# Performance work log

Measured on AMD Instinct MI355X. Metric: run time of the kernel, lower is better.

The kernel has to match this reference:

```python
import jax, jax.numpy as jnp
import numpy as np

B, S, H, D = 2, 2048, 16, 64
HID = H * D
THETA = 10000.0
SCALING_FACTOR = 1
NEG_INF = -1e9


def _rope_cos_sin(position_ids):
    # Llama RoPE: inv_freq over even dims, duplicated halves.
    inv_freq = 1.0 / (THETA ** (jnp.arange(0, D, 2, dtype=jnp.float32) / D))  # [D/2]
    freqs = position_ids.astype(jnp.float32)[..., None] * inv_freq            # [B,S,D/2]
    emb = jnp.concatenate([freqs, freqs], axis=-1)                            # [B,S,D]
    return jnp.cos(emb), jnp.sin(emb)


def _rotate_half(x):
    x1, x2 = jnp.split(x, 2, axis=-1)
    return jnp.concatenate([-x2, x1], axis=-1)


def setup_inputs() -> dict:
    key = jax.random.key(0)
    ks = jax.random.split(key, 6)
    return {
        "hidden_states": jax.random.normal(ks[0], (B, S, HID), dtype=jnp.float32),
        "info_embeddings": jax.random.normal(ks[1], (B, S, HID), dtype=jnp.float32) * 0.1,
        "Wq": jax.random.normal(ks[2], (HID, HID), dtype=jnp.float32) * 0.02,
        "Wk": jax.random.normal(ks[3], (HID, HID), dtype=jnp.float32) * 0.02,
        "Wv": jax.random.normal(ks[4], (HID, HID), dtype=jnp.float32) * 0.02,
        "Wo": jax.random.normal(ks[5], (HID, HID), dtype=jnp.float32) * 0.02,
        "position_ids": jnp.broadcast_to(jnp.arange(S, dtype=jnp.int64), (B, S)),
    }


def reference(hidden_states, info_embeddings, Wq, Wk, Wv, Wo, position_ids):
    b, s, _ = hidden_states.shape
    # projections -> [B,H,S,D]
    q = (hidden_states @ Wq).reshape(b, s, H, D).transpose(0, 2, 1, 3)
    k = (hidden_states @ Wk).reshape(b, s, H, D).transpose(0, 2, 1, 3)
    v = (hidden_states @ Wv).reshape(b, s, H, D).transpose(0, 2, 1, 3)
    # info embedding added to q and k (pre-RoPE)
    info = info_embeddings.reshape(b, s, H, D).transpose(0, 2, 1, 3)
    q = q + info
    k = k + info
    # rotary position embedding
    cos, sin = _rope_cos_sin(position_ids)
    cos = cos[:, None]  # [B,1,S,D]
    sin = sin[:, None]
    q = q * cos + _rotate_half(q) * sin
    k = k * cos + _rotate_half(k) * sin
    # eager attention with custom scaling
    scale = 1.0 / float(np.sqrt(SCALING_FACTOR * D))
    scores = jnp.einsum("bhqd,bhkd->bhqk", q, k) * scale  # [B,H,S,S]
    causal = jnp.tril(jnp.ones((s, s), dtype=bool))
    scores = scores + jnp.where(causal, 0.0, NEG_INF).astype(scores.dtype)
    probs = jax.nn.softmax(scores, axis=-1)  # dropout p=0 (eval)
    attn = jnp.einsum("bhqk,bhkd->bhqd", probs, v)
    attn = attn.transpose(0, 2, 1, 3).reshape(b, s, HID)
    return attn @ Wo
```

## Files before the change

### kernel.cpp

```cpp
#include <hip/hip_runtime.h>
#include <hip/hip_bf16.h>

#define HB 2
#define HS 2048
#define HH 16
#define HD 64
#define HIDN 1024
#define MROWS 4096

typedef __attribute__((ext_vector_type(8))) short s16x8;
typedef __attribute__((ext_vector_type(4))) float f32x4;
typedef unsigned short u16;

__device__ inline u16 f2bf(float f) {
  union { __hip_bfloat16 h; u16 u; } cvt;
  cvt.h = __float2bfloat16(f);
  return cvt.u;
}

__device__ __forceinline__ void gload16(const u16* g, u16* l) {
  __builtin_amdgcn_global_load_lds((const __attribute__((address_space(1))) void*)g,
                                   (__attribute__((address_space(3))) void*)l, 16, 0, 0);
}

__global__ __launch_bounds__(256) void k_cvt(const float* __restrict__ in, u16* __restrict__ out, int n) {
  int i = (blockIdx.x * 256 + threadIdx.x) * 4;
  if (i >= n) return;
  float4 a = *(const float4*)(in + i);
  ushort4 r;
  r.x = f2bf(a.x); r.y = f2bf(a.y); r.z = f2bf(a.z); r.w = f2bf(a.w);
  *(ushort4*)(out + i) = r;
}

__global__ __launch_bounds__(256) void k_transpose(const float* __restrict__ W0, const float* __restrict__ W1,
                                                   const float* __restrict__ W2, const float* __restrict__ W3,
                                                   u16* __restrict__ out) {
  const float* W = (blockIdx.z == 0) ? W0 : (blockIdx.z == 1) ? W1 : (blockIdx.z == 2) ? W2 : W3;
  u16* O = out + (size_t)blockIdx.z * HIDN * HIDN;
  __shared__ float tile[64][65];
  int k0 = blockIdx.y * 64, c0 = blockIdx.x * 64;
  #pragma unroll
  for (int i = 0; i < 16; ++i) {
    int id = threadIdx.x + i * 256;
    int r = id >> 6, c = id & 63;
    tile[r][c] = W[(size_t)(k0 + r) * HIDN + c0 + c];
  }
  __syncthreads();
  #pragma unroll
  for (int i = 0; i < 16; ++i) {
    int id = threadIdx.x + i * 256;
    int r = id >> 6, c = id & 63;
    O[(size_t)(c0 + r) * HIDN + k0 + c] = f2bf(tile[c][r]);
  }
}

#define BM 128
#define BN 128
#define BK 64
#define LDK 72

__global__ __launch_bounds__(256) void k_qkv(const u16* __restrict__ X, const u16* __restrict__ Wt,
                                             const float* __restrict__ info,
                                             u16* __restrict__ Qb, u16* __restrict__ Kb, u16* __restrict__ Vt) {
  __shared__ __align__(16) u16 smem[128 * 136];
  const int z = blockIdx.z;
  const u16* Bt = Wt + (size_t)z * HIDN * HIDN;
  const int tid = threadIdx.x;
  const int lane = tid & 63, wave = tid >> 6;
  const int wr = wave >> 1, wc = wave & 1;
  const int lg = lane >> 4, li = lane & 15;
  const int bm0 = blockIdx.y * BM, bn0 = blockIdx.x * BN;

  const int srow = lane >> 3;
  const int scol = (lane & 7) * 8;

  f32x4 acc[4][4];
  #pragma unroll
  for (int m = 0; m < 4; ++m)
    #pragma unroll
    for (int n = 0; n < 4; ++n) acc[m][n] = (f32x4){0.f, 0.f, 0.f, 0.f};

  for (int k0 = 0; k0 < HIDN; k0 += BK) {
    __syncthreads();
    #pragma unroll
    for (int c = 0; c < 4; ++c) {
      const int ci = wave * 4 + c;
      const int row = ci * 8 + srow;
      gload16(X  + (size_t)(bm0 + row) * HIDN + k0 + scol, &smem[ci * 512]);
      gload16(Bt + (size_t)(bn0 + row) * HIDN + k0 + scol, &smem[8192 + ci * 512]);
    }
    __syncthreads();
    #pragma unroll
    for (int kk = 0; kk < 2; ++kk) {
      s16x8 af[4], bfr[4];
      #pragma unroll
      for (int m = 0; m < 4; ++m) af[m]  = *(const s16x8*)(&smem[(wr * 64 + m * 16 + li) * 64 + kk * 32 + lg * 8]);
      #pragma unroll
      for (int n = 0; n < 4; ++n) bfr[n] = *(const s16x8*)(&smem[8192 + (wc * 64 + n * 16 + li) * 64 + kk * 32 + lg * 8]);
      __builtin_amdgcn_s_setprio(1);
      #pragma unroll
      for (int m = 0; m < 4; ++m)
        #pragma unroll
        for (int n = 0; n < 4; ++n)
          acc[m][n] = __builtin_amdgcn_mfma_f32_16x16x32_bf16(af[m], bfr[n], acc[m][n], 0, 0, 0);
      __builtin_amdgcn_s_setprio(0);
    }
  }

  if (z < 2) {
    u16* dst = (z == 0) ? Qb : Kb;
    #pragma unroll
    for (int m = 0; m < 4; ++m) {
      #pragma unroll
      for (int r = 0; r < 4; ++r) {
        int t = bm0 + wr * 64 + m * 16 + lg * 4 + r;
        int b = t >> 11, s = t & (HS - 1);
        #pragma unroll
        for (int n = 0; n < 2; ++n) {
          int c1 = bn0 + wc * 64 + n * 16 + li;
          float v1 = acc[m][n][r]     + info[(size_t)t * HIDN + c1];
          float v2 = acc[m][n + 2][r] + info[(size_t)t * HIDN + c1 + 32];
          int j = n * 16 + li;
          float invf = exp2f(-0.41524101186092030f * (float)j);
          float ang = (float)s * invf;
          float sn, cs;
          __sincosf(ang, &sn, &cs);
          float o1 = v1 * cs - v2 * sn;
          float o2 = v2 * cs + v1 * sn;
          if (z == 0) { o1 *= 0.18033688011f; o2 *= 0.18033688011f; }
          int h = c1 >> 6, d1 = c1 & 63;
          size_t base = ((size_t)(b * HH + h) * HS + s) * HD;
          dst[base + d1]      = f2bf(o1);
          dst[base + d1 + 32] = f2bf(o2);
        }
      }
    }
  } else {
    __syncthreads();
    #pragma unroll
    for (int m = 0; m < 4; ++m)
      #pragma unroll
      for (int n = 0; n < 4; ++n)
        #pragma unroll
        for (int r = 0; r < 4; ++r) {
          int cl = wc * 64 + n * 16 + li;
          int ml = wr * 64 + m * 16 + lg * 4 + r;
          smem[cl * 136 + ml] = f2bf(acc[m][n][r]);
        }
    __syncthreads();
    const int b = bm0 >> 11, s0 = bm0 & (HS - 1);
    #pragma unroll
    for (int p = 0; p < 8; ++p) {
      int id = tid + p * 256;
      int cl = id >> 4, m8 = (id & 15) * 8;
      int c = bn0 + cl;
      int h = c >> 6, d = c & 63;
      s16x8 v = *(const s16x8*)(&smem[cl * 136 + m8]);
      *(s16x8*)(&Vt[((size_t)(b * HH + h) * HD + d) * HS + s0 + m8]) = v;
    }
  }
}

__global__ __launch_bounds__(512, 4) void k_attn(const u16* __restrict__ Qb, const u16* __restrict__ Kb,
                                                 const u16* __restrict__ Vt, u16* __restrict__ attnOut) {
  __shared__ u16 Ks[2][64 * LDK];
  __shared__ u16 Vs[2][64 * LDK];
  __shared__ u16 Ps[8][16 * LDK];
  const int bidx = blockIdx.x;
  const int bh = bidx & 31;
  const int x  = bidx >> 5;
  const int j  = (x < 8) ? x : 23 - x;
  const int q0 = j * 128;
  const int ntiles = 2 * j + 2;

  const u16* Qh = Qb + (size_t)bh * HS * HD;
  const u16* Kh = Kb + (size_t)bh * HS * HD;
  const u16* Vh = Vt + (size_t)bh * HD * HS;
  const int tid = threadIdx.x;
  const int lane = tid & 63, w = tid >> 6;
  const int lg = lane >> 4, li = lane & 15;
  const int b = bh >> 4, h = bh & 15;

  const int row8 = lane >> 3;
  const int col8 = (lane & 7) * 8;

  s16x8 qf[2];
  #pragma unroll
  for (int kk = 0; kk < 2; ++kk)
    qf[kk] = *(const s16x8*)(Qh + (size_t)(q0 + w * 16 + li) * HD + kk * 32 + lg * 8);

  f32x4 o[4];
  #pragma unroll
  for (int n = 0; n < 4; ++n) o[n] = (f32x4){0.f, 0.f, 0.f, 0.f};
  float mrow = -3e38f, lrow = 0.f;

  {
    uint4 rK = *(const uint4*)(Kh + (size_t)(w * 8 + row8) * HD + col8);
    uint4 rV = *(const uint4*)(Vh + (size_t)(w * 8 + row8) * HS + col8);
    *(uint4*)(&Ks[0][(w * 8 + row8) * LDK + col8]) = rK;
    *(uint4*)(&Vs[0][(w * 8 + row8) * LDK + col8]) = rV;
  }
  __syncthreads();

  for (int t = 0; t < ntiles; ++t) {
    const int cur = t & 1;
    uint4 rK, rV;
    const bool more = (t + 1 < ntiles);
    if (more) {
      const int kv1 = (t + 1) * 64;
      rK = *(const uint4*)(Kh + (size_t)(kv1 + w * 8 + row8) * HD + col8);
      rV = *(const uint4*)(Vh + (size_t)(w * 8 + row8) * HS + kv1 + col8);
    }

    f32x4 sc[4];
    #pragma unroll
    for (int n = 0; n < 4; ++n) sc[n] = (f32x4){0.f, 0.f, 0.f, 0.f};
    __builtin_amdgcn_s_setprio(1);
    #pragma unroll
    for (int kk = 0; kk < 2; ++kk) {
      #pragma unroll
      for (int n = 0; n < 4; ++n) {
        s16x8 kfr = *(const s16x8*)(&Ks[cur][(n * 16 + li) * LDK + kk * 32 + lg * 8]);
        sc[n] = __builtin_amdgcn_mfma_f32_16x16x32_bf16(kfr, qf[kk], sc[n], 0, 0, 0);
      }
    }
    __builtin_amdgcn_s_setprio(0);

    if (t >= 2 * j) {
      const int qglob = q0 + w * 16 + li;
      #pragma unroll
      for (int n = 0; n < 4; ++n)
        #pragma unroll
        for (int r = 0; r < 4; ++r)
          if (t * 64 + n * 16 + lg * 4 + r > qglob) sc[n][r] = -1e9f;
    }

    float pmax = sc[0][0];
    #pragma unroll
    for (int n = 0; n < 4; ++n)
      #pragma unroll
      for (int r = 0; r < 4; ++r) pmax = fmaxf(pmax, sc[n][r]);
    pmax = fmaxf(pmax, __shfl_xor(pmax, 16));
    pmax = fmaxf(pmax, __shfl_xor(pmax, 32));

    if (!__all(pmax - mrow <= 11.5f)) {
      float mnew = fmaxf(mrow, pmax);
      float corr = exp2f(mrow - mnew);
      mrow = mnew;
      lrow *= corr;
      float corrq[4];
      #pragma unroll
      for (int r = 0; r < 4; ++r) corrq[r] = __shfl(corr, lg * 4 + r);
      #pragma unroll
      for (int n = 0; n < 4; ++n)
        #pragma unroll
        for (int r = 0; r < 4; ++r) o[n][r] *= corrq[r];
    }

    float psum = 0.f;
    #pragma unroll
    for (int n = 0; n < 4; ++n) {
      u16 pb[4];
      #pragma unroll
      for (int r = 0; r < 4; ++r) {
        float p = exp2f(sc[n][r] - mrow);
        psum += p;
        pb[r] = f2bf(p);
      }
      uint2 wv;
      wv.x = (unsigned)pb[0] | ((unsigned)pb[1] << 16);
      wv.y = (unsigned)pb[2] | ((unsigned)pb[3] << 16);
      *(uint2*)(&Ps[w][li * LDK + n * 16 + lg * 4]) = wv;
    }
    psum += __shfl_xor(psum, 16);
    psum += __shfl_xor(psum, 32);
    lrow += psum;

    __builtin_amdgcn_s_setprio(1);
    #pragma unroll
    for (int kk = 0; kk < 2; ++kk) {
      s16x8 pf = *(const s16x8*)(&Ps[w][li * LDK + kk * 32 + lg * 8]);
      #pragma unroll
      for (int n = 0; n < 4; ++n) {
        s16x8 vf = *(const s16x8*)(&Vs[cur][(n * 16 + li) * LDK + kk * 32 + lg * 8]);
        o[n] = __builtin_amdgcn_mfma_f32_16x16x32_bf16(pf, vf, o[n], 0, 0, 0);
      }
    }
    __builtin_amdgcn_s_setprio(0);

    if (more) {
      *(uint4*)(&Ks[cur ^ 1][(w * 8 + row8) * LDK + col8]) = rK;
      *(uint4*)(&Vs[cur ^ 1][(w * 8 + row8) * LDK + col8]) = rV;
      __syncthreads();
    }
  }

  float linv = 1.0f / lrow;
  float linvq[4];
  #pragma unroll
  for (int r = 0; r < 4; ++r) linvq[r] = __shfl(linv, lg * 4 + r);
  #pragma unroll
  for (int n = 0; n < 4; ++n)
    #pragma unroll
    for (int r = 0; r < 4; ++r) {
      int srow = q0 + w * 16 + lg * 4 + r;
      attnOut[(size_t)(b * HS + srow) * HIDN + h * 64 + n * 16 + li] = f2bf(o[n][r] * linvq[r]);
    }
}

__global__ __launch_bounds__(256) void k_out(const u16* __restrict__ A, const u16* __restrict__ Bt,
                                             float* __restrict__ out) {
  __shared__ __align__(16) u16 As[BM * 64];
  __shared__ __align__(16) u16 Bs[BN * 64];
  const int tid = threadIdx.x;
  const int lane = tid & 63, wave = tid >> 6;
  const int wr = wave >> 1, wc = wave & 1;
  const int lg = lane >> 4, li = lane & 15;
  const int bm0 = blockIdx.y * BM, bn0 = blockIdx.x * BN;

  const int srow = lane >> 3;
  const int scol = (lane & 7) * 8;

  f32x4 acc[4][4];
  #pragma unroll
  for (int m = 0; m < 4; ++m)
    #pragma unroll
    for (int n = 0; n < 4; ++n) acc[m][n] = (f32x4){0.f, 0.f, 0.f, 0.f};

  for (int k0 = 0; k0 < HIDN; k0 += BK) {
    __syncthreads();
    #pragma unroll
    for (int c = 0; c < 4; ++c) {
      const int ci = wave * 4 + c;
      const int row = ci * 8 + srow;
      gload16(A  + (size_t)(bm0 + row) * HIDN + k0 + scol, &As[ci * 512]);
      gload16(Bt + (size_t)(bn0 + row) * HIDN + k0 + scol, &Bs[ci * 512]);
    }
    __syncthreads();
    #pragma unroll
    for (int kk = 0; kk < 2; ++kk) {
      s16x8 af[4], bfr[4];
      #pragma unroll
      for (int m = 0; m < 4; ++m) af[m]  = *(const s16x8*)(&As[(wr * 64 + m * 16 + li) * 64 + kk * 32 + lg * 8]);
      #pragma unroll
      for (int n = 0; n < 4; ++n) bfr[n] = *(const s16x8*)(&Bs[(wc * 64 + n * 16 + li) * 64 + kk * 32 + lg * 8]);
      __builtin_amdgcn_s_setprio(1);
      #pragma unroll
      for (int m = 0; m < 4; ++m)
        #pragma unroll
        for (int n = 0; n < 4; ++n)
          acc[m][n] = __builtin_amdgcn_mfma_f32_16x16x32_bf16(af[m], bfr[n], acc[m][n], 0, 0, 0);
      __builtin_amdgcn_s_setprio(0);
    }
  }

  #pragma unroll
  for (int m = 0; m < 4; ++m)
    #pragma unroll
    for (int r = 0; r < 4; ++r) {
      int t = bm0 + wr * 64 + m * 16 + lg * 4 + r;
      #pragma unroll
      for (int n = 0; n < 4; ++n) {
        int c = bn0 + wc * 64 + n * 16 + li;
        out[(size_t)t * HIDN + c] = acc[m][n][r];
      }
    }
}

extern "C" void kernel_launch(void* const* d_in, const int* in_sizes, int n_in,
                              void* d_out, int out_size, void* d_ws, size_t ws_size,
                              hipStream_t stream) {
  const float* hs   = (const float*)d_in[0];
  const float* info = (const float*)d_in[1];
  const float* Wq   = (const float*)d_in[2];
  const float* Wk   = (const float*)d_in[3];
  const float* Wv   = (const float*)d_in[4];
  const float* Wo   = (const float*)d_in[5];
  float* out = (float*)d_out;

  char* ws = (char*)d_ws;
  u16* Xbf  = (u16*)(ws);
  u16* Wt   = (u16*)(ws + ((size_t)8  << 20));
  u16* Qb   = (u16*)(ws + ((size_t)16 << 20));
  u16* Kb   = (u16*)(ws + ((size_t)24 << 20));
  u16* Vt   = (u16*)(ws + ((size_t)32 << 20));
  u16* attn = Xbf;

  k_cvt<<<(MROWS * HIDN / 4 + 255) / 256, 256, 0, stream>>>(hs, Xbf, MROWS * HIDN);
  k_transpose<<<dim3(16, 16, 4), 256, 0, stream>>>(Wq, Wk, Wv, Wo, Wt);
  k_qkv<<<dim3(HIDN / BN, MROWS / BM, 3), 256, 0, stream>>>(Xbf, Wt, info, Qb, Kb, Vt);
  k_attn<<<dim3(512), 512, 0, stream>>>(Qb, Kb, Vt, attn);
  k_out<<<dim3(HIDN / BN, MROWS / BM), 256, 0, stream>>>(attn, Wt + (size_t)3 * HIDN * HIDN, out);
}
```

Before: 129.2 us.

## Split attention into 64-row query blocks with 256 threads, heaviest-first ordering

The attention kernel now uses 256-thread blocks, each covering 64 query rows, with 1024 blocks launched in descending-work order in place of the paired 128-row scheme. Each thread loads two K and V rows per tile, and the causal mask applies only to the diagonal tile. The fp32-to-bf16 conversion of probabilities is replaced by a round-half-up add plus a byte permute. This aims at better load balance and occupancy across CUs. The cost is K/V tiles being reloaded by twice as many blocks, and slightly different rounding, since ties and NaN are not handled like round-to-nearest-even.

```diff
diff --git a/kernel.cpp b/kernel.cpp
--- a/kernel.cpp
+++ b/kernel.cpp
@@ -161,17 +161,16 @@
   }
 }
 
-__global__ __launch_bounds__(512, 4) void k_attn(const u16* __restrict__ Qb, const u16* __restrict__ Kb,
+__global__ __launch_bounds__(256, 3) void k_attn(const u16* __restrict__ Qb, const u16* __restrict__ Kb,
                                                  const u16* __restrict__ Vt, u16* __restrict__ attnOut) {
   __shared__ u16 Ks[2][64 * LDK];
   __shared__ u16 Vs[2][64 * LDK];
-  __shared__ u16 Ps[8][16 * LDK];
+  __shared__ u16 Ps[4][16 * LDK];
   const int bidx = blockIdx.x;
   const int bh = bidx & 31;
-  const int x  = bidx >> 5;
-  const int j  = (x < 8) ? x : 23 - x;
-  const int q0 = j * 128;
-  const int ntiles = 2 * j + 2;
+  const int j  = 31 - (bidx >> 5);
+  const int q0 = j * 64;
+  const int ntiles = j + 1;
 
   const u16* Qh = Qb + (size_t)bh * HS * HD;
   const u16* Kh = Kb + (size_t)bh * HS * HD;
@@ -181,8 +180,8 @@
   const int lg = lane >> 4, li = lane & 15;
   const int b = bh >> 4, h = bh & 15;
 
-  const int row8 = lane >> 3;
-  const int col8 = (lane & 7) * 8;
+  const int row16 = tid >> 3;
+  const int col8  = (tid & 7) * 8;
 
   s16x8 qf[2];
   #pragma unroll
@@ -195,21 +194,27 @@
   float mrow = -3e38f, lrow = 0.f;
 
   {
-    uint4 rK = *(const uint4*)(Kh + (size_t)(w * 8 + row8) * HD + col8);
-    uint4 rV = *(const uint4*)(Vh + (size_t)(w * 8 + row8) * HS + col8);
-    *(uint4*)(&Ks[0][(w * 8 + row8) * LDK + col8]) = rK;
-    *(uint4*)(&Vs[0][(w * 8 + row8) * LDK + col8]) = rV;
+    uint4 ka = *(const uint4*)(Kh + (size_t)row16 * HD + col8);
+    uint4 kb = *(const uint4*)(Kh + (size_t)(row16 + 32) * HD + col8);
+    uint4 va = *(const uint4*)(Vh + (size_t)row16 * HS + col8);
+    uint4 vb = *(const uint4*)(Vh + (size_t)(row16 + 32) * HS + col8);
+    *(uint4*)(&Ks[0][row16 * LDK + col8])        = ka;
+    *(uint4*)(&Ks[0][(row16 + 32) * LDK + col8]) = kb;
+    *(uint4*)(&Vs[0][row16 * LDK + col8])        = va;
+    *(uint4*)(&Vs[0][(row16 + 32) * LDK + col8]) = vb;
   }
   __syncthreads();
 
   for (int t = 0; t < ntiles; ++t) {
     const int cur = t & 1;
-    uint4 rK, rV;
+    uint4 rKa, rKb, rVa, rVb;
     const bool more = (t + 1 < ntiles);
     if (more) {
       const int kv1 = (t + 1) * 64;
-      rK = *(const uint4*)(Kh + (size_t)(kv1 + w * 8 + row8) * HD + col8);
-      rV = *(const uint4*)(Vh + (size_t)(w * 8 + row8) * HS + kv1 + col8);
+      rKa = *(const uint4*)(Kh + (size_t)(kv1 + row16) * HD + col8);
+      rKb = *(const uint4*)(Kh + (size_t)(kv1 + row16 + 32) * HD + col8);
+      rVa = *(const uint4*)(Vh + (size_t)row16 * HS + kv1 + col8);
+      rVb = *(const uint4*)(Vh + (size_t)(row16 + 32) * HS + kv1 + col8);
     }
 
     f32x4 sc[4];
@@ -226,13 +231,13 @@
     }
     __builtin_amdgcn_s_setprio(0);
 
-    if (t >= 2 * j) {
-      const int qglob = q0 + w * 16 + li;
+    if (t == ntiles - 1) {
+      const int qrel = w * 16 + li;
       #pragma unroll
       for (int n = 0; n < 4; ++n)
         #pragma unroll
         for (int r = 0; r < 4; ++r)
-          if (t * 64 + n * 16 + lg * 4 + r > qglob) sc[n][r] = -1e9f;
+          if (n * 16 + lg * 4 + r > qrel) sc[n][r] = -1e9f;
     }
 
     float pmax = sc[0][0];
@@ -260,16 +265,18 @@
     float psum = 0.f;
     #pragma unroll
     for (int n = 0; n < 4; ++n) {
-      u16 pb[4];
-      #pragma unroll
-      for (int r = 0; r < 4; ++r) {
-        float p = exp2f(sc[n][r] - mrow);
-        psum += p;
-        pb[r] = f2bf(p);
-      }
+      float p0 = exp2f(sc[n][0] - mrow);
+      float p1 = exp2f(sc[n][1] - mrow);
+      float p2 = exp2f(sc[n][2] - mrow);
+      float p3 = exp2f(sc[n][3] - mrow);
+      psum += (p0 + p1) + (p2 + p3);
+      unsigned a0 = __float_as_uint(p0) + 0x8000u;
+      unsigned a1 = __float_as_uint(p1) + 0x8000u;
+      unsigned a2 = __float_as_uint(p2) + 0x8000u;
+      unsigned a3 = __float_as_uint(p3) + 0x8000u;
       uint2 wv;
-      wv.x = (unsigned)pb[0] | ((unsigned)pb[1] << 16);
-      wv.y = (unsigned)pb[2] | ((unsigned)pb[3] << 16);
+      wv.x = __builtin_amdgcn_perm(a1, a0, 0x07060302u);
+      wv.y = __builtin_amdgcn_perm(a3, a2, 0x07060302u);
       *(uint2*)(&Ps[w][li * LDK + n * 16 + lg * 4]) = wv;
     }
     psum += __shfl_xor(psum, 16);
@@ -289,8 +296,10 @@
     __builtin_amdgcn_s_setprio(0);
 
     if (more) {
-      *(uint4*)(&Ks[cur ^ 1][(w * 8 + row8) * LDK + col8]) = rK;
-      *(uint4*)(&Vs[cur ^ 1][(w * 8 + row8) * LDK + col8]) = rV;
+      *(uint4*)(&Ks[cur ^ 1][row16 * LDK + col8])        = rKa;
+      *(uint4*)(&Ks[cur ^ 1][(row16 + 32) * LDK + col8]) = rKb;
+      *(uint4*)(&Vs[cur ^ 1][row16 * LDK + col8])        = rVa;
+      *(uint4*)(&Vs[cur ^ 1][(row16 + 32) * LDK + col8]) = rVb;
       __syncthreads();
     }
   }
@@ -389,6 +398,6 @@
   k_cvt<<<(MROWS * HIDN / 4 + 255) / 256, 256, 0, stream>>>(hs, Xbf, MROWS * HIDN);
   k_transpose<<<dim3(16, 16, 4), 256, 0, stream>>>(Wq, Wk, Wv, Wo, Wt);
   k_qkv<<<dim3(HIDN / BN, MROWS / BM, 3), 256, 0, stream>>>(Xbf, Wt, info, Qb, Kb, Vt);
-  k_attn<<<dim3(512), 512, 0, stream>>>(Qb, Kb, Vt, attn);
+  k_attn<<<dim3(1024), 256, 0, stream>>>(Qb, Kb, Vt, attn);
   k_out<<<dim3(HIDN / BN, MROWS / BM), 256, 0, stream>>>(attn, Wt + (size_t)3 * HIDN * HIDN, out);
 }
```

Measured after the change: 125.1 us. -3.2%, faster.
